# Performance work log

Measured on AMD Instinct MI355X. Metric: run time of the kernel, lower is better.

## Reference

```python
import jax, jax.numpy as jnp
import numpy as np

def setup_inputs() -> dict:
    key = jax.random.key(0)
    k1, k2, k3, k4, k5 = jax.random.split(key, 5)
    B, Lc, Lq, D = 32, 512, 64, 1024
    return {
        "c": jax.random.normal(k1, (B, Lc, D), dtype=jnp.float32),
        "q": jax.random.normal(k2, (B, Lq, D), dtype=jnp.float32),
        "proj_c": jax.random.normal(k3, (D, 1), dtype=jnp.float32) * 0.04,
        "proj_q": jax.random.normal(k4, (D, 1), dtype=jnp.float32) * 0.04,
        "proj_cq": jax.random.normal(k5, (1, 1, D), dtype=jnp.float32) * 0.04,
    }

def reference(c, q, proj_c, proj_q, proj_cq):
    # similarity: s0 + s1 + s2, shape [B, Lc, Lq]
    s0 = c @ proj_c                                   # [B, Lc, 1]
    s1 = jnp.swapaxes(q @ proj_q, 1, 2)               # [B, 1, Lq]
    s2 = jnp.einsum('bcd,bqd->bcq', c * proj_cq, q)   # [B, Lc, Lq]
    sim = s0 + s1 + s2

    # context-to-query attention
    a_c2q = jax.nn.softmax(sim, axis=-1)              # [B, Lc, Lq]
    c2q = jnp.einsum('bcq,bqd->bcd', a_c2q, q)        # [B, Lc, D]

    # query-to-context attention (max over query dim, softmax over context)
    a_q2c = jax.nn.softmax(jnp.max(sim, axis=-1), axis=-1)  # [B, Lc]
    q2c = jnp.einsum('bc,bcd->bd', a_q2c, c)[:, None, :]    # [B, 1, D], broadcasts over Lc

    out = jnp.concatenate((c, c2q, c * q2c, c * c2q), axis=-1)  # [B, Lc, 4D]
    return out
```

## Files before the change

kernel.cpp:

```cpp
#include <hip/hip_runtime.h>

#define B 32
#define LC 512
#define LQ 64
#define DD 1024


typedef __attribute__((ext_vector_type(8))) short bf16x8;
typedef __attribute__((ext_vector_type(4))) float f32x4;

__device__ inline short f2bf(float f) {
    unsigned u = __builtin_bit_cast(unsigned, f);
    u += 0x7FFFu + ((u >> 16) & 1u);
    return (short)(u >> 16);
}

__device__ inline bf16x8 pack8(float4 a, float4 b) {
    bf16x8 r;
    r[0] = f2bf(a.x); r[1] = f2bf(a.y); r[2] = f2bf(a.z); r[3] = f2bf(a.w);
    r[4] = f2bf(b.x); r[5] = f2bf(b.y); r[6] = f2bf(b.z); r[7] = f2bf(b.w);
    return r;
}

__device__ inline float dot4(float4 a, float4 b) {
    return a.x * b.x + a.y * b.y + a.z * b.z + a.w * b.w;
}

__global__ __launch_bounds__(256) void k1_sim(const float* __restrict__ c,
                                              const float* __restrict__ q,
                                              const float* __restrict__ proj_c,
                                              const float* __restrict__ proj_q,
                                              const float* __restrict__ proj_cq,
                                              short* __restrict__ P,
                                              float* __restrict__ mfull) {
    const int b  = blockIdx.x >> 4;
    const int i0 = (blockIdx.x & 15) * 32;
    const int t  = threadIdx.x;
    const int w  = t >> 6, lane = t & 63;
    const int l15 = lane & 15, quad = lane >> 4;

    __shared__ __align__(16) short sA[32][72];
    __shared__ __align__(16) short sB[64][72];
    __shared__ float rmaxL[32][4];
    __shared__ float rsumL[32][4];
    __shared__ float s0red[32][8];
    __shared__ float s1red[64][4];
    __shared__ float s1L[64];

    const int arow = t >> 3, ag = t & 7;
    const int brow = t >> 2, bg = t & 3;

    const float* cbase = c + (size_t)(b * LC + i0 + arow) * DD + ag * 8;
    const float* qbase = q + (size_t)(b * LQ + brow) * DD + bg * 16;

    f32x4 acc[2] = {{0.f,0.f,0.f,0.f},{0.f,0.f,0.f,0.f}};
    float s0p = 0.f, s1p = 0.f;

    float4 a0 = *(const float4*)(cbase + 0);
    float4 a1 = *(const float4*)(cbase + 4);
    float4 b0 = *(const float4*)(qbase + 0);
    float4 b1 = *(const float4*)(qbase + 4);
    float4 b2 = *(const float4*)(qbase + 8);
    float4 b3 = *(const float4*)(qbase + 12);

    for (int kc = 0; kc < 16; ++kc) {
        float4 na0, na1, nb0, nb1, nb2, nb3;
        if (kc < 15) {
            const float* cn = cbase + (kc + 1) * 64;
            const float* qn = qbase + (kc + 1) * 64;
            na0 = *(const float4*)(cn + 0);
            na1 = *(const float4*)(cn + 4);
            nb0 = *(const float4*)(qn + 0);
            nb1 = *(const float4*)(qn + 4);
            nb2 = *(const float4*)(qn + 8);
            nb3 = *(const float4*)(qn + 12);
        }
        {
            const float* pcq = proj_cq + kc * 64 + ag * 8;
            const float* pc  = proj_c  + kc * 64 + ag * 8;
            const float* pq  = proj_q  + kc * 64 + bg * 16;
            float4 p0 = *(const float4*)(pcq + 0);
            float4 p1 = *(const float4*)(pcq + 4);
            float4 c0 = *(const float4*)(pc + 0);
            float4 c1 = *(const float4*)(pc + 4);
            float4 pq0 = *(const float4*)(pq + 0);
            float4 pq1 = *(const float4*)(pq + 4);
            float4 pq2 = *(const float4*)(pq + 8);
            float4 pq3 = *(const float4*)(pq + 12);
            s0p += dot4(a0, c0) + dot4(a1, c1);
            s1p += dot4(b0, pq0) + dot4(b1, pq1) + dot4(b2, pq2) + dot4(b3, pq3);
            float4 m0 = {a0.x * p0.x, a0.y * p0.y, a0.z * p0.z, a0.w * p0.w};
            float4 m1 = {a1.x * p1.x, a1.y * p1.y, a1.z * p1.z, a1.w * p1.w};
            *(bf16x8*)&sA[arow][ag * 8] = pack8(m0, m1);
            *(bf16x8*)&sB[brow][bg * 16 + 0] = pack8(b0, b1);
            *(bf16x8*)&sB[brow][bg * 16 + 8] = pack8(b2, b3);
        }
        __syncthreads();
#pragma unroll
        for (int s = 0; s < 2; ++s) {
            int ko = s * 32 + quad * 8;
            bf16x8 bf = *(const bf16x8*)&sB[w * 16 + l15][ko];
#pragma unroll
            for (int mt = 0; mt < 2; ++mt) {
                bf16x8 af = *(const bf16x8*)&sA[mt * 16 + l15][ko];
                acc[mt] = __builtin_amdgcn_mfma_f32_16x16x32_bf16(af, bf, acc[mt], 0, 0, 0);
            }
        }
        __syncthreads();
        if (kc < 15) { a0 = na0; a1 = na1; b0 = nb0; b1 = nb1; b2 = nb2; b3 = nb3; }
    }

    s0red[arow][ag] = s0p;
    s1red[brow][bg] = s1p;
    __syncthreads();
    if (t < 64) s1L[t] = s1red[t][0] + s1red[t][1] + s1red[t][2] + s1red[t][3];
    __syncthreads();

    const float s1j = s1L[w * 16 + l15];
    float v[2][4];
#pragma unroll
    for (int mt = 0; mt < 2; ++mt) {
#pragma unroll
        for (int r = 0; r < 4; ++r) {
            float vv = acc[mt][r] + s1j;
            v[mt][r] = vv;
            float rm = vv;
#pragma unroll
            for (int off = 1; off < 16; off <<= 1) rm = fmaxf(rm, __shfl_xor(rm, off, 16));
            if (l15 == 0) rmaxL[mt * 16 + quad * 4 + r][w] = rm;
        }
    }
    __syncthreads();
    float e[2][4];
#pragma unroll
    for (int mt = 0; mt < 2; ++mt) {
#pragma unroll
        for (int r = 0; r < 4; ++r) {
            int row = mt * 16 + quad * 4 + r;
            float m = fmaxf(fmaxf(rmaxL[row][0], rmaxL[row][1]),
                            fmaxf(rmaxL[row][2], rmaxL[row][3]));
            float ee = __expf(v[mt][r] - m);
            e[mt][r] = ee;
            float se = ee;
#pragma unroll
            for (int off = 1; off < 16; off <<= 1) se += __shfl_xor(se, off, 16);
            if (l15 == 0) rsumL[row][w] = se;
        }
    }
    __syncthreads();
#pragma unroll
    for (int mt = 0; mt < 2; ++mt) {
#pragma unroll
        for (int r = 0; r < 4; ++r) {
            int row = mt * 16 + quad * 4 + r;
            float s = rsumL[row][0] + rsumL[row][1] + rsumL[row][2] + rsumL[row][3];
            P[(size_t)(b * LC + i0 + row) * LQ + w * 16 + l15] = f2bf(e[mt][r] / s);
        }
    }
    if (t < 32) {
        float s0v = 0.f;
#pragma unroll
        for (int k = 0; k < 8; ++k) s0v += s0red[t][k];
        float mm = fmaxf(fmaxf(rmaxL[t][0], rmaxL[t][1]),
                         fmaxf(rmaxL[t][2], rmaxL[t][3]));
        mfull[b * LC + i0 + t] = mm + s0v;
    }
}

__global__ __launch_bounds__(256) void k2_q2c(const float* __restrict__ c,
                                              const float* __restrict__ mfull,
                                              float* __restrict__ q2c) {
    const int b  = blockIdx.x >> 3;
    const int d0 = (blockIdx.x & 7) * 128;
    const int t  = threadIdx.x;
    __shared__ float aL[LC];
    __shared__ float redm[4];
    __shared__ float reds[4];

    float m0 = mfull[b * LC + t];
    float m1 = mfull[b * LC + 256 + t];
    float mx = fmaxf(m0, m1);
#pragma unroll
    for (int off = 32; off; off >>= 1) mx = fmaxf(mx, __shfl_xor(mx, off, 64));
    if ((t & 63) == 0) redm[t >> 6] = mx;
    __syncthreads();
    float bm = fmaxf(fmaxf(redm[0], redm[1]), fmaxf(redm[2], redm[3]));
    float e0 = __expf(m0 - bm), e1 = __expf(m1 - bm);
    float s = e0 + e1;
#pragma unroll
    for (int off = 32; off; off >>= 1) s += __shfl_xor(s, off, 64);
    if ((t & 63) == 0) reds[t >> 6] = s;
    __syncthreads();
    float bs = reds[0] + reds[1] + reds[2] + reds[3];
    float inv = 1.0f / bs;
    aL[t] = e0 * inv;
    aL[t + 256] = e1 * inv;
    __syncthreads();

    const int tx = t & 31, ty = t >> 5;
    float4 acc = {0.f, 0.f, 0.f, 0.f};
    const float* cb = c + (size_t)b * LC * DD + d0 + tx * 4;
    for (int i = ty; i < LC; i += 8) {
        float a = aL[i];
        float4 cv = *(const float4*)(cb + (size_t)i * DD);
        acc.x += a * cv.x; acc.y += a * cv.y; acc.z += a * cv.z; acc.w += a * cv.w;
    }
    __shared__ __align__(16) float4 red[8][32];
    red[ty][tx] = acc;
    __syncthreads();
    if (t < 32) {
        float4 sv = red[0][t];
#pragma unroll
        for (int k = 1; k < 8; ++k) {
            float4 v2 = red[k][t];
            sv.x += v2.x; sv.y += v2.y; sv.z += v2.z; sv.w += v2.w;
        }
        *(float4*)(q2c + b * DD + d0 + t * 4) = sv;
    }
}

__global__ __launch_bounds__(256) void k3_out(const float* __restrict__ c,
                                              const float* __restrict__ q,
                                              const short* __restrict__ P,
                                              const float* __restrict__ q2c,
                                              float* __restrict__ out) {
    const int b  = blockIdx.x >> 5;
    const int i0 = ((blockIdx.x >> 1) & 15) * 32;
    const int h  = blockIdx.x & 1;
    const int t  = threadIdx.x;
    const int w  = t >> 6, lane = t & 63;
    const int l15 = lane & 15, quad = lane >> 4;

    __shared__ __align__(16) short sBq[64][72];
    __shared__ __align__(16) float ct[32][68];

    bf16x8 paf[2][2];
#pragma unroll
    for (int s = 0; s < 2; ++s)
#pragma unroll
        for (int mt = 0; mt < 2; ++mt)
            paf[s][mt] = *(const bf16x8*)&P[(size_t)(b * LC + i0 + mt * 16 + l15) * LQ
                                           + s * 32 + quad * 8];

    const int j0 = (t & 31) * 2, dg = t >> 5;
    const int erow = t >> 4, ed = (t & 15) * 4;

    const int dcb = h * 8;
    const float* qb0 = q + (size_t)(b * LQ + j0) * DD + dg * 8 + dcb * 64;
    const float* qb1 = qb0 + DD;

    float4 r0 = *(const float4*)(qb0 + 0);
    float4 r1 = *(const float4*)(qb0 + 4);
    float4 r2 = *(const float4*)(qb1 + 0);
    float4 r3 = *(const float4*)(qb1 + 4);

    for (int dci = 0; dci < 8; ++dci) {
        const int d0 = (dcb + dci) * 64;
        float4 n0, n1, n2, n3;
        if (dci < 7) {
            n0 = *(const float4*)(qb0 + (dci + 1) * 64);
            n1 = *(const float4*)(qb0 + (dci + 1) * 64 + 4);
            n2 = *(const float4*)(qb1 + (dci + 1) * 64);
            n3 = *(const float4*)(qb1 + (dci + 1) * 64 + 4);
        }
        float4 cc0 = *(const float4*)(c + (size_t)(b * LC + i0 + erow) * DD + d0 + ed);
        float4 cc1 = *(const float4*)(c + (size_t)(b * LC + i0 + erow + 16) * DD + d0 + ed);
        float4 g2  = *(const float4*)(q2c + b * DD + d0 + ed);

        const float* fr0 = (const float*)&r0;
        const float* fr1 = (const float*)&r1;
        const float* fr2 = (const float*)&r2;
        const float* fr3 = (const float*)&r3;
#pragma unroll
        for (int e = 0; e < 8; ++e) {
            float v0 = (e < 4) ? fr0[e] : fr1[e - 4];
            float v1 = (e < 4) ? fr2[e] : fr3[e - 4];
            unsigned pk = (unsigned)(unsigned short)f2bf(v0)
                        | ((unsigned)(unsigned short)f2bf(v1) << 16);
            *(unsigned*)&sBq[dg * 8 + e][j0] = pk;
        }
        __syncthreads();

        f32x4 acc2[2] = {{0.f,0.f,0.f,0.f},{0.f,0.f,0.f,0.f}};
#pragma unroll
        for (int s = 0; s < 2; ++s) {
            int ko = s * 32 + quad * 8;
            bf16x8 bf = *(const bf16x8*)&sBq[w * 16 + l15][ko];
#pragma unroll
            for (int mt = 0; mt < 2; ++mt)
                acc2[mt] = __builtin_amdgcn_mfma_f32_16x16x32_bf16(paf[s][mt], bf, acc2[mt], 0, 0, 0);
        }
#pragma unroll
        for (int mt = 0; mt < 2; ++mt)
#pragma unroll
            for (int r = 0; r < 4; ++r)
                ct[mt * 16 + quad * 4 + r][w * 16 + l15] = acc2[mt][r];
        __syncthreads();

#pragma unroll
        for (int k = 0; k < 2; ++k) {
            int row = erow + 16 * k;
            float4 cc = k ? cc1 : cc0;
            float4 cqv = *(const float4*)&ct[row][ed];
            float* ob = out + (size_t)(b * LC + i0 + row) * (4 * DD) + d0 + ed;
            *(float4*)(ob) = cc;
            *(float4*)(ob + DD) = cqv;
            float4 o2 = {cc.x * g2.x, cc.y * g2.y, cc.z * g2.z, cc.w * g2.w};
            *(float4*)(ob + 2 * DD) = o2;
            float4 o3 = {cc.x * cqv.x, cc.y * cqv.y, cc.z * cqv.z, cc.w * cqv.w};
            *(float4*)(ob + 3 * DD) = o3;
        }
        if (dci < 7) { r0 = n0; r1 = n1; r2 = n2; r3 = n3; }
    }
}

extern "C" void kernel_launch(void* const* d_in, const int* in_sizes, int n_in,
                              void* d_out, int out_size, void* d_ws, size_t ws_size,
                              hipStream_t stream) {
    const float* c       = (const float*)d_in[0];
    const float* q       = (const float*)d_in[1];
    const float* proj_c  = (const float*)d_in[2];
    const float* proj_q  = (const float*)d_in[3];
    const float* proj_cq = (const float*)d_in[4];
    float* out = (float*)d_out;
    float* ws  = (float*)d_ws;

    float* mfull = ws;
    float* q2c   = ws + 16384;
    short* P     = (short*)(ws + 49152);

    hipLaunchKernelGGL(k1_sim, dim3(512),  dim3(256), 0, stream,
                       c, q, proj_c, proj_q, proj_cq, P, mfull);
    hipLaunchKernelGGL(k2_q2c, dim3(256),  dim3(256), 0, stream, c, mfull, q2c);
    hipLaunchKernelGGL(k3_out, dim3(1024), dim3(256), 0, stream, c, q, P, q2c, out);
}
```

Measured before the change: 379.6 us.

## Precompute bf16 q and its transpose once, swizzle block order across XCDs

```diff
diff --git a/kernel.cpp b/kernel.cpp
--- a/kernel.cpp
+++ b/kernel.cpp
@@ -26,15 +26,82 @@
     return a.x * b.x + a.y * b.y + a.z * b.z + a.w * b.w;
 }
 
+__device__ inline int xswz(int bid, int nwg) {
+    return (bid & 7) * (nwg >> 3) + (bid >> 3);
+}
+
+__global__ __launch_bounds__(256) void k0_q(const float* __restrict__ q,
+                                            const float* __restrict__ proj_q,
+                                            short* __restrict__ qbf,
+                                            short* __restrict__ qT,
+                                            float* __restrict__ s1part) {
+    const int bid = xswz(blockIdx.x, 512);
+    const int b  = bid >> 4;
+    const int d0 = (bid & 15) * 64;
+    const int sl = bid & 15;
+    const int t  = threadIdx.x;
+
+    __shared__ __align__(16) short tile[64][72];
+    __shared__ float s1red[64][8];
+
+    const int j0 = (t & 31) * 2;
+    const int dg = t >> 5;
+
+    const float* qr0 = q + (size_t)(b * LQ + j0) * DD + d0 + dg * 8;
+    const float* qr1 = qr0 + DD;
+    float4 x0 = *(const float4*)(qr0 + 0);
+    float4 x1 = *(const float4*)(qr0 + 4);
+    float4 y0 = *(const float4*)(qr1 + 0);
+    float4 y1 = *(const float4*)(qr1 + 4);
+    float4 p0 = *(const float4*)(proj_q + d0 + dg * 8);
+    float4 p1 = *(const float4*)(proj_q + d0 + dg * 8 + 4);
+
+    s1red[j0][dg]     = dot4(x0, p0) + dot4(x1, p1);
+    s1red[j0 + 1][dg] = dot4(y0, p0) + dot4(y1, p1);
+
+    *(bf16x8*)&qbf[(size_t)(b * LQ + j0) * DD + d0 + dg * 8]     = pack8(x0, x1);
+    *(bf16x8*)&qbf[(size_t)(b * LQ + j0 + 1) * DD + d0 + dg * 8] = pack8(y0, y1);
+
+    const float* fx0 = (const float*)&x0;
+    const float* fx1 = (const float*)&x1;
+    const float* fy0 = (const float*)&y0;
+    const float* fy1 = (const float*)&y1;
+#pragma unroll
+    for (int e = 0; e < 8; ++e) {
+        float v0 = (e < 4) ? fx0[e] : fx1[e - 4];
+        float v1 = (e < 4) ? fy0[e] : fy1[e - 4];
+        unsigned pk = (unsigned)(unsigned short)f2bf(v0)
+                    | ((unsigned)(unsigned short)f2bf(v1) << 16);
+        *(unsigned*)&tile[dg * 8 + e][j0] = pk;
+    }
+    __syncthreads();
+
+    {
+        const int d = t >> 2, part = t & 3;
+        bf16x8 v0 = *(const bf16x8*)&tile[d][part * 16];
+        bf16x8 v1 = *(const bf16x8*)&tile[d][part * 16 + 8];
+        short* dst = qT + ((size_t)b * DD + d0 + d) * LQ + part * 16;
+        *(bf16x8*)(dst)     = v0;
+        *(bf16x8*)(dst + 8) = v1;
+    }
+    if (t < 64) {
+        float s = 0.f;
+#pragma unroll
+        for (int k = 0; k < 8; ++k) s += s1red[t][k];
+        s1part[(b * 16 + sl) * 64 + t] = s;
+    }
+}
+
 __global__ __launch_bounds__(256) void k1_sim(const float* __restrict__ c,
-                                              const float* __restrict__ q,
+                                              const short* __restrict__ qbf,
                                               const float* __restrict__ proj_c,
-                                              const float* __restrict__ proj_q,
                                               const float* __restrict__ proj_cq,
+                                              const float* __restrict__ s1part,
                                               short* __restrict__ P,
                                               float* __restrict__ mfull) {
-    const int b  = blockIdx.x >> 4;
-    const int i0 = (blockIdx.x & 15) * 32;
+    const int bid = xswz(blockIdx.x, 512);
+    const int b  = bid >> 4;
+    const int i0 = (bid & 15) * 32;
     const int t  = threadIdx.x;
     const int w  = t >> 6, lane = t & 63;
     const int l15 = lane & 15, quad = lane >> 4;
@@ -44,56 +111,46 @@
     __shared__ float rmaxL[32][4];
     __shared__ float rsumL[32][4];
     __shared__ float s0red[32][8];
-    __shared__ float s1red[64][4];
     __shared__ float s1L[64];
 
     const int arow = t >> 3, ag = t & 7;
     const int brow = t >> 2, bg = t & 3;
 
     const float* cbase = c + (size_t)(b * LC + i0 + arow) * DD + ag * 8;
-    const float* qbase = q + (size_t)(b * LQ + brow) * DD + bg * 16;
+    const short* qbase = qbf + (size_t)(b * LQ + brow) * DD + bg * 16;
 
     f32x4 acc[2] = {{0.f,0.f,0.f,0.f},{0.f,0.f,0.f,0.f}};
-    float s0p = 0.f, s1p = 0.f;
+    float s0p = 0.f;
 
     float4 a0 = *(const float4*)(cbase + 0);
     float4 a1 = *(const float4*)(cbase + 4);
-    float4 b0 = *(const float4*)(qbase + 0);
-    float4 b1 = *(const float4*)(qbase + 4);
-    float4 b2 = *(const float4*)(qbase + 8);
-    float4 b3 = *(const float4*)(qbase + 12);
+    bf16x8 u0 = *(const bf16x8*)(qbase + 0);
+    bf16x8 u1 = *(const bf16x8*)(qbase + 8);
 
     for (int kc = 0; kc < 16; ++kc) {
-        float4 na0, na1, nb0, nb1, nb2, nb3;
+        float4 na0, na1;
+        bf16x8 nu0, nu1;
         if (kc < 15) {
             const float* cn = cbase + (kc + 1) * 64;
-            const float* qn = qbase + (kc + 1) * 64;
+            const short* qn = qbase + (kc + 1) * 64;
             na0 = *(const float4*)(cn + 0);
             na1 = *(const float4*)(cn + 4);
-            nb0 = *(const float4*)(qn + 0);
-            nb1 = *(const float4*)(qn + 4);
-            nb2 = *(const float4*)(qn + 8);
-            nb3 = *(const float4*)(qn + 12);
+            nu0 = *(const bf16x8*)(qn + 0);
+            nu1 = *(const bf16x8*)(qn + 8);
         }
         {
             const float* pcq = proj_cq + kc * 64 + ag * 8;
             const float* pc  = proj_c  + kc * 64 + ag * 8;
-            const float* pq  = proj_q  + kc * 64 + bg * 16;
             float4 p0 = *(const float4*)(pcq + 0);
             float4 p1 = *(const float4*)(pcq + 4);
             float4 c0 = *(const float4*)(pc + 0);
             float4 c1 = *(const float4*)(pc + 4);
-            float4 pq0 = *(const float4*)(pq + 0);
-            float4 pq1 = *(const float4*)(pq + 4);
-            float4 pq2 = *(const float4*)(pq + 8);
-            float4 pq3 = *(const float4*)(pq + 12);
             s0p += dot4(a0, c0) + dot4(a1, c1);
-            s1p += dot4(b0, pq0) + dot4(b1, pq1) + dot4(b2, pq2) + dot4(b3, pq3);
             float4 m0 = {a0.x * p0.x, a0.y * p0.y, a0.z * p0.z, a0.w * p0.w};
             float4 m1 = {a1.x * p1.x, a1.y * p1.y, a1.z * p1.z, a1.w * p1.w};
             *(bf16x8*)&sA[arow][ag * 8] = pack8(m0, m1);
-            *(bf16x8*)&sB[brow][bg * 16 + 0] = pack8(b0, b1);
-            *(bf16x8*)&sB[brow][bg * 16 + 8] = pack8(b2, b3);
+            *(bf16x8*)&sB[brow][bg * 16 + 0] = u0;
+            *(bf16x8*)&sB[brow][bg * 16 + 8] = u1;
         }
         __syncthreads();
 #pragma unroll
@@ -107,13 +164,16 @@
             }
         }
         __syncthreads();
-        if (kc < 15) { a0 = na0; a1 = na1; b0 = nb0; b1 = nb1; b2 = nb2; b3 = nb3; }
+        if (kc < 15) { a0 = na0; a1 = na1; u0 = nu0; u1 = nu1; }
     }
 
     s0red[arow][ag] = s0p;
-    s1red[brow][bg] = s1p;
-    __syncthreads();
-    if (t < 64) s1L[t] = s1red[t][0] + s1red[t][1] + s1red[t][2] + s1red[t][3];
+    if (t < 64) {
+        float s = 0.f;
+#pragma unroll
+        for (int k = 0; k < 16; ++k) s += s1part[(b * 16 + k) * 64 + t];
+        s1L[t] = s;
+    }
     __syncthreads();
 
     const float s1j = s1L[w * 16 + l15];
@@ -170,8 +230,9 @@
 __global__ __launch_bounds__(256) void k2_q2c(const float* __restrict__ c,
                                               const float* __restrict__ mfull,
                                               float* __restrict__ q2c) {
-    const int b  = blockIdx.x >> 3;
-    const int d0 = (blockIdx.x & 7) * 128;
+    const int bid = xswz(blockIdx.x, 256);
+    const int b  = bid >> 3;
+    const int d0 = (bid & 7) * 128;
     const int t  = threadIdx.x;
     __shared__ float aL[LC];
     __shared__ float redm[4];
@@ -220,19 +281,19 @@
 }
 
 __global__ __launch_bounds__(256) void k3_out(const float* __restrict__ c,
-                                              const float* __restrict__ q,
+                                              const short* __restrict__ qT,
                                               const short* __restrict__ P,
                                               const float* __restrict__ q2c,
                                               float* __restrict__ out) {
-    const int b  = blockIdx.x >> 5;
-    const int i0 = ((blockIdx.x >> 1) & 15) * 32;
-    const int h  = blockIdx.x & 1;
+    const int bid = xswz(blockIdx.x, 2048);
+    const int b  = bid >> 6;
+    const int i0 = ((bid >> 2) & 15) * 32;
+    const int qd = bid & 3;
     const int t  = threadIdx.x;
     const int w  = t >> 6, lane = t & 63;
     const int l15 = lane & 15, quad = lane >> 4;
 
-    __shared__ __align__(16) short sBq[64][72];
-    __shared__ __align__(16) float ct[32][68];
+    __shared__ __align__(16) short sBq[256][72];
 
     bf16x8 paf[2][2];
 #pragma unroll
@@ -242,75 +303,46 @@
             paf[s][mt] = *(const bf16x8*)&P[(size_t)(b * LC + i0 + mt * 16 + l15) * LQ
                                            + s * 32 + quad * 8];
 
-    const int j0 = (t & 31) * 2, dg = t >> 5;
-    const int erow = t >> 4, ed = (t & 15) * 4;
-
-    const int dcb = h * 8;
-    const float* qb0 = q + (size_t)(b * LQ + j0) * DD + dg * 8 + dcb * 64;
-    const float* qb1 = qb0 + DD;
-
-    float4 r0 = *(const float4*)(qb0 + 0);
-    float4 r1 = *(const float4*)(qb0 + 4);
-    float4 r2 = *(const float4*)(qb1 + 0);
-    float4 r3 = *(const float4*)(qb1 + 4);
-
-    for (int dci = 0; dci < 8; ++dci) {
-        const int d0 = (dcb + dci) * 64;
-        float4 n0, n1, n2, n3;
-        if (dci < 7) {
-            n0 = *(const float4*)(qb0 + (dci + 1) * 64);
-            n1 = *(const float4*)(qb0 + (dci + 1) * 64 + 4);
-            n2 = *(const float4*)(qb1 + (dci + 1) * 64);
-            n3 = *(const float4*)(qb1 + (dci + 1) * 64 + 4);
-        }
-        float4 cc0 = *(const float4*)(c + (size_t)(b * LC + i0 + erow) * DD + d0 + ed);
-        float4 cc1 = *(const float4*)(c + (size_t)(b * LC + i0 + erow + 16) * DD + d0 + ed);
-        float4 g2  = *(const float4*)(q2c + b * DD + d0 + ed);
-
-        const float* fr0 = (const float*)&r0;
-        const float* fr1 = (const float*)&r1;
-        const float* fr2 = (const float*)&r2;
-        const float* fr3 = (const float*)&r3;
-#pragma unroll
-        for (int e = 0; e < 8; ++e) {
-            float v0 = (e < 4) ? fr0[e] : fr1[e - 4];
-            float v1 = (e < 4) ? fr2[e] : fr3[e - 4];
-            unsigned pk = (unsigned)(unsigned short)f2bf(v0)
-                        | ((unsigned)(unsigned short)f2bf(v1) << 16);
-            *(unsigned*)&sBq[dg * 8 + e][j0] = pk;
-        }
-        __syncthreads();
-
+    {
+        const short* src = qT + ((size_t)b * DD + qd * 256) * LQ;
+#pragma unroll
+        for (int it = 0; it < 8; ++it) {
+            int f = it * 256 + t;
+            bf16x8 vv = *(const bf16x8*)(src + f * 8);
+            *(bf16x8*)&sBq[f >> 3][(f & 7) * 8] = vv;
+        }
+    }
+    __syncthreads();
+
+    const float* cb  = c + (size_t)(b * LC + i0) * DD + qd * 256;
+    const float* g2b = q2c + b * DD + qd * 256;
+    float* ob = out + (size_t)(b * LC + i0) * (4 * DD) + qd * 256;
+
+    for (int dci = 0; dci < 4; ++dci) {
+        const int dl = dci * 64 + w * 16 + l15;
+        float g2 = g2b[dl];
         f32x4 acc2[2] = {{0.f,0.f,0.f,0.f},{0.f,0.f,0.f,0.f}};
 #pragma unroll
         for (int s = 0; s < 2; ++s) {
-            int ko = s * 32 + quad * 8;
-            bf16x8 bf = *(const bf16x8*)&sBq[w * 16 + l15][ko];
+            bf16x8 bf = *(const bf16x8*)&sBq[dl][s * 32 + quad * 8];
 #pragma unroll
             for (int mt = 0; mt < 2; ++mt)
                 acc2[mt] = __builtin_amdgcn_mfma_f32_16x16x32_bf16(paf[s][mt], bf, acc2[mt], 0, 0, 0);
         }
 #pragma unroll
-        for (int mt = 0; mt < 2; ++mt)
-#pragma unroll
-            for (int r = 0; r < 4; ++r)
-                ct[mt * 16 + quad * 4 + r][w * 16 + l15] = acc2[mt][r];
-        __syncthreads();
-
-#pragma unroll
-        for (int k = 0; k < 2; ++k) {
-            int row = erow + 16 * k;
-            float4 cc = k ? cc1 : cc0;
-            float4 cqv = *(const float4*)&ct[row][ed];
-            float* ob = out + (size_t)(b * LC + i0 + row) * (4 * DD) + d0 + ed;
-            *(float4*)(ob) = cc;
-            *(float4*)(ob + DD) = cqv;
-            float4 o2 = {cc.x * g2.x, cc.y * g2.y, cc.z * g2.z, cc.w * g2.w};
-            *(float4*)(ob + 2 * DD) = o2;
-            float4 o3 = {cc.x * cqv.x, cc.y * cqv.y, cc.z * cqv.z, cc.w * cqv.w};
-            *(float4*)(ob + 3 * DD) = o3;
-        }
-        if (dci < 7) { r0 = n0; r1 = n1; r2 = n2; r3 = n3; }
+        for (int mt = 0; mt < 2; ++mt) {
+#pragma unroll
+            for (int r = 0; r < 4; ++r) {
+                int row = mt * 16 + quad * 4 + r;
+                float cc = cb[(size_t)row * DD + dl];
+                float cqv = acc2[mt][r];
+                float* o = ob + (size_t)row * (4 * DD) + dl;
+                o[0]      = cc;
+                o[DD]     = cqv;
+                o[2 * DD] = cc * g2;
+                o[3 * DD] = cc * cqv;
+            }
+        }
     }
 }
 
@@ -325,12 +357,16 @@
     float* out = (float*)d_out;
     float* ws  = (float*)d_ws;
 
-    float* mfull = ws;
-    float* q2c   = ws + 16384;
-    short* P     = (short*)(ws + 49152);
-
+    float* mfull  = ws;
+    float* q2c    = ws + 16384;
+    float* s1part = ws + 49152;
+    short* P      = (short*)(ws + 81920);
+    short* qbf    = (short*)(ws + 606208);
+    short* qT     = (short*)(ws + 1654784);
+
+    hipLaunchKernelGGL(k0_q,   dim3(512),  dim3(256), 0, stream, q, proj_q, qbf, qT, s1part);
     hipLaunchKernelGGL(k1_sim, dim3(512),  dim3(256), 0, stream,
-                       c, q, proj_c, proj_q, proj_cq, P, mfull);
+                       c, qbf, proj_c, proj_cq, s1part, P, mfull);
     hipLaunchKernelGGL(k2_q2c, dim3(256),  dim3(256), 0, stream, c, mfull, q2c);
-    hipLaunchKernelGGL(k3_out, dim3(1024), dim3(256), 0, stream, c, q, P, q2c, out);
-}
+    hipLaunchKernelGGL(k3_out, dim3(2048), dim3(256), 0, stream, c, qT, P, q2c, out);
+}
```

After: 390.2 us. 1.03x slower.
